# Kernel tuning notes

Hardware: AMD Instinct MI355X
Metric: run time of the kernel (lower is better)

Reference implementation:

```python
import jax, jax.numpy as jnp
import numpy as np

N_Q = 4       # n_qubits
PATCH = 3
PAD = 1       # patch_size // 2


def _u3(theta, phi, lam):
    # U3 gate matrix (2x2 complex)
    c = jnp.cos(theta / 2)
    s = jnp.sin(theta / 2)
    row0 = jnp.stack([c + 0j, -jnp.exp(1j * lam) * s])
    row1 = jnp.stack([jnp.exp(1j * phi) * s, jnp.exp(1j * (phi + lam)) * c])
    return jnp.stack([row0, row1]).astype(jnp.complex64)


def _apply_1q(state, U, wire):
    # state: (N,2,2,2,2) complex; U: (2,2) shared or (N,2,2) batched
    s = jnp.moveaxis(state, 1 + wire, -1)
    shp = s.shape
    s = s.reshape(s.shape[0], -1, 2)
    if U.ndim == 2:
        out = jnp.einsum('ij,nrj->nri', U, s)
    else:
        out = jnp.einsum('nij,nrj->nri', U, s)
    return jnp.moveaxis(out.reshape(shp), -1, 1 + wire)


def _apply_2q(state, U4, cw, tw):
    # U4: (4,4) on (control, target) subspace ordered |c t>
    s = jnp.moveaxis(state, (1 + cw, 1 + tw), (-2, -1))
    shp = s.shape
    s = s.reshape(s.shape[0], -1, 4)
    out = jnp.einsum('ij,nrj->nri', U4, s)
    return jnp.moveaxis(out.reshape(shp), (-2, -1), (1 + cw, 1 + tw))


def setup_inputs() -> dict:
    key = jax.random.key(0)
    ks = jax.random.split(key, 8)
    B, C, H, W = 16, 64, 64, 64
    out_ch = 128
    d_in = C * PATCH * PATCH  # 576
    x = jax.random.normal(ks[0], (B, C, H, W), dtype=jnp.float32)
    fc1_w = jax.random.normal(ks[1], (N_Q, d_in), dtype=jnp.float32) * (1.0 / np.sqrt(d_in))
    fc1_b = jax.random.normal(ks[2], (N_Q,), dtype=jnp.float32) * 0.01
    u3_params = jax.random.normal(ks[3], (N_Q, 3), dtype=jnp.float32)
    cu3_params = jax.random.normal(ks[4], (N_Q, 3), dtype=jnp.float32)
    fc_w = jax.random.normal(ks[5], (out_ch, N_Q), dtype=jnp.float32) * 0.5
    fc_b = jax.random.normal(ks[6], (out_ch,), dtype=jnp.float32) * 0.01
    return {"x": x, "fc1_w": fc1_w, "fc1_b": fc1_b, "u3_params": u3_params,
            "cu3_params": cu3_params, "fc_w": fc_w, "fc_b": fc_b}


def reference(x, fc1_w, fc1_b, u3_params, cu3_params, fc_w, fc_b):
    B, C, H, W = x.shape
    xp = jnp.pad(x, ((0, 0), (0, 0), (PAD, PAD), (PAD, PAD)))
    Hout, Wout = H, W  # stride 1, same padding
    # im2col: feature order (C, di, dj) matches torch patch.reshape(B,-1)
    cols = jnp.stack([xp[:, :, di:di + Hout, dj:dj + Wout]
                      for di in range(PATCH) for dj in range(PATCH)], axis=2)  # (B,C,9,H,W)
    patches = cols.transpose(0, 3, 4, 1, 2).reshape(B, Hout * Wout, C * PATCH * PATCH)
    ang = patches @ fc1_w.T + fc1_b  # (B, P, 4) rotation angles
    Np = B * Hout * Wout
    ang = ang.reshape(Np, N_Q)
    # initial state |0000> for every (batch, patch)
    state = jnp.zeros((Np, 2 ** N_Q), jnp.complex64).at[:, 0].set(1.0)
    state = state.reshape((Np,) + (2,) * N_Q)
    # RY encoding (per-element angles)
    for w in range(N_Q):
        th = ang[:, w] / 2
        c, s = jnp.cos(th), jnp.sin(th)
        Ury = jnp.stack([jnp.stack([c, -s], -1), jnp.stack([s, c], -1)], -2).astype(jnp.complex64)
        state = _apply_1q(state, Ury, w)
    # trainable U3 on every wire
    for w in range(N_Q):
        state = _apply_1q(state, _u3(u3_params[w, 0], u3_params[w, 1], u3_params[w, 2]), w)
    # circular CU3 ring (0,1),(1,2),(2,3),(3,0)
    for w in range(N_Q):
        U = _u3(cu3_params[w, 0], cu3_params[w, 1], cu3_params[w, 2])
        U4 = jnp.eye(4, dtype=jnp.complex64).at[2:, 2:].set(U)
        state = _apply_2q(state, U4, w, (w + 1) % N_Q)
    # <Z> on each wire
    probs = state.real ** 2 + state.imag ** 2  # (Np,2,2,2,2)
    zv = jnp.array([1.0, -1.0], jnp.float32)
    expz = jnp.stack(
        [(probs * zv.reshape((1,) + (1,) * w + (2,) + (1,) * (N_Q - 1 - w))).sum(axis=(1, 2, 3, 4))
         for w in range(N_Q)], axis=1)  # (Np,4)
    out = expz.reshape(B, Hout * Wout, N_Q) @ fc_w.T + fc_b  # (B,P,out_ch)
    out_ch = fc_w.shape[0]
    # faithful to original: view(B, out_ch, side_h, side_w) on contiguous (P,out_ch)
    return out.reshape(B, out_ch, Hout, Wout)
```

## Files before the change

### kernel.cpp

```cpp
#include <hip/hip_runtime.h>
#include <hip/hip_bf16.h>
#include <math.h>

typedef unsigned short u16;
typedef unsigned int   u32;
typedef unsigned long long u64;

#define WS_W2    0
#define WS_B4    2304
#define WS_FCW   2308
#define WS_FCB   2820
#define WS_GATES 2948
#define WS_FLAG  3012
#define WS_PART  4096

__device__ inline float bfbits2f(u32 lo16) {
    u32 u = lo16 << 16;
    return __builtin_bit_cast(float, u);
}
__device__ inline float bchi(u32 w) {
    return __builtin_bit_cast(float, w & 0xffff0000u);
}
__device__ inline float bclo(u32 w) {
    return __builtin_bit_cast(float, w << 16);
}
__device__ inline u16 f2bf(float f) {
    u32 u = __builtin_bit_cast(u32, f);
    u = u + 0x7fffu + ((u >> 16) & 1u);
    return (u16)(u >> 16);
}
__device__ inline float ld_param(const void* p, int i, int isbf16) {
    return isbf16 ? bfbits2f(((const u16*)p)[i]) : ((const float*)p)[i];
}

__global__ __launch_bounds__(256) void k0_prep(
        const void* __restrict__ x,
        const void* __restrict__ fc1_w, const void* __restrict__ fc1_b,
        const void* __restrict__ u3p,   const void* __restrict__ cu3p,
        const void* __restrict__ fc_w,  const void* __restrict__ fc_b,
        float* __restrict__ ws) {
    __shared__ int sflag;
    int t = threadIdx.x;
    if (t == 0) {
        const u32* xw = (const u32*)x;
        int cnt = 0;
        for (int i = 0; i < 64; ++i) {
            u32 e = (xw[i] >> 7) & 0xFFu;
            if (e >= 110 && e <= 130) ++cnt;
        }
        sflag = (cnt >= 32) ? 1 : 0;
        ws[WS_FLAG] = (float)sflag;
    }
    __syncthreads();
    const int bf = sflag;
    for (int idx = t; idx < 2304; idx += 256) {
        int c = idx / 36;
        int rem = idx - c * 36;
        int q = rem / 9;
        int k = rem - q * 9;
        ws[WS_W2 + idx] = ld_param(fc1_w, q * 576 + c * 9 + k, bf);
    }
    if (t < 4)   ws[WS_B4 + t] = ld_param(fc1_b, t, bf);
    for (int idx = t; idx < 512; idx += 256) ws[WS_FCW + idx] = ld_param(fc_w, idx, bf);
    if (t < 128) ws[WS_FCB + t] = ld_param(fc_b, t, bf);
    if (t < 8) {
        int w = t & 3;
        const void* p = (t < 4) ? u3p : cu3p;
        float th = ld_param(p, w * 3 + 0, bf);
        float ph = ld_param(p, w * 3 + 1, bf);
        float la = ld_param(p, w * 3 + 2, bf);
        float c = cosf(0.5f * th), s = sinf(0.5f * th);
        float cl = cosf(la), sl = sinf(la);
        float cp = cosf(ph), sp = sinf(ph);
        float cpl = cp * cl - sp * sl, spl = sp * cl + cp * sl;
        float* m = ws + WS_GATES + t * 8;
        m[0] = c;        m[1] = 0.f;
        m[2] = -cl * s;  m[3] = -sl * s;
        m[4] = cp * s;   m[5] = sp * s;
        m[6] = cpl * c;  m[7] = spl * c;
    }
}

__global__ __launch_bounds__(256) void kA_conv(
        const void* __restrict__ x, const float* __restrict__ ws,
        float4* __restrict__ part) {
    __shared__ u32 tile[3 * 16 * 34];
    __shared__ float4 red4[256];
    const int t = threadIdx.x;
    const int bid = blockIdx.x;
    const int cg  = bid & 3;
    const int row = (bid >> 2) & 63;
    const int b   = bid >> 8;
    const int bf = (ws[WS_FLAG] != 0.0f) ? 1 : 0;
    const int c0 = cg * 16;

    const u32*    xu = (const u32*)x;
    const float2* xf = (const float2*)x;
    const int xbase = b * 131072;

    {
        const int jj = t & 31;
        const int half = t >> 5;
#pragma unroll
        for (int i = 0; i < 6; ++i) {
            int rowcl = half + i * 8;
            int r = rowcl >> 4, cl = rowcl & 15;
            int gr = row - 1 + r;
            u32 pk = 0;
            if (gr >= 0 && gr < 64) {
                int idx = xbase + (c0 + cl) * 2048 + gr * 32 + jj;
                if (bf) pk = xu[idx];
                else { float2 v = xf[idx];
                       pk = (u32)f2bf(v.x) | ((u32)f2bf(v.y) << 16); }
            }
            tile[rowcl * 34 + 1 + jj] = pk;
        }
        if (t < 96) { int rc = t >> 1; tile[rc * 34 + ((t & 1) ? 33 : 0)] = 0u; }
    }
    __syncthreads();

    const int j = t & 63, tc = t >> 6;
    const int pj = (j + 1) >> 1;
    const int sh = (1 - (j & 1)) * 16;
    float ang0 = 0.f, ang1 = 0.f, ang2 = 0.f, ang3 = 0.f;
#pragma unroll
    for (int cc = 0; cc < 4; ++cc) {
        const int cl = tc * 4 + cc;
        const int cs = __builtin_amdgcn_readfirstlane(c0 + cl);
        const float* wp = ws + WS_W2 + cs * 36;
#pragma unroll
        for (int r = 0; r < 3; ++r) {
            const u32* rp = tile + (r * 16 + cl) * 34 + pj;
            u32 lo = rp[0], hi = rp[1];
            u64 v = (((u64)hi << 32) | lo) >> sh;
            u32 vlo = (u32)v, vhi = (u32)(v >> 32);
            float e0 = bclo(vlo);
            float e1 = bchi(vlo);
            float e2 = bclo(vhi);
            const float* w0 = wp + r * 3;
            ang0 += e0 * w0[0]  + e1 * w0[1]  + e2 * w0[2];
            ang1 += e0 * w0[9]  + e1 * w0[10] + e2 * w0[11];
            ang2 += e0 * w0[18] + e1 * w0[19] + e2 * w0[20];
            ang3 += e0 * w0[27] + e1 * w0[28] + e2 * w0[29];
        }
    }

    red4[tc * 64 + j] = make_float4(ang0, ang1, ang2, ang3);
    __syncthreads();
    if (t < 64) {
        float4 a0 = red4[t], a1 = red4[64 + t], a2 = red4[128 + t], a3 = red4[192 + t];
        float4 s = make_float4(a0.x + a1.x + a2.x + a3.x,
                               a0.y + a1.y + a2.y + a3.y,
                               a0.z + a1.z + a2.z + a3.z,
                               a0.w + a1.w + a2.w + a3.w);
        part[cg * 65536 + b * 4096 + row * 64 + t] = s;
    }
}

__global__ __launch_bounds__(256) void kB_circuit_fc(
        const float* __restrict__ ws, const float4* __restrict__ part,
        void* __restrict__ out) {
    __shared__ float4 smEz[64];
    const int t = threadIdx.x;
    const int bp0 = blockIdx.x * 64;
    const int bf = (ws[WS_FLAG] != 0.0f) ? 1 : 0;

    if (t < 64) {
        const int bp = bp0 + t;
        float4 a0 = part[bp];
        float4 a1 = part[65536 + bp];
        float4 a2 = part[131072 + bp];
        float4 a3 = part[196608 + bp];
        float angf[4];
        angf[0] = ws[WS_B4 + 0] + a0.x + a1.x + a2.x + a3.x;
        angf[1] = ws[WS_B4 + 1] + a0.y + a1.y + a2.y + a3.y;
        angf[2] = ws[WS_B4 + 2] + a0.z + a1.z + a2.z + a3.z;
        angf[3] = ws[WS_B4 + 3] + a0.w + a1.w + a2.w + a3.w;

        const float* G = ws + WS_GATES;
        float vr[4][2], vi[4][2];
#pragma unroll
        for (int w = 0; w < 4; ++w) {
            float sa, ca;
            __sincosf(0.5f * angf[w], &sa, &ca);
            const float* m = G + w * 8;
            vr[w][0] = m[0] * ca + m[2] * sa;  vi[w][0] = m[1] * ca + m[3] * sa;
            vr[w][1] = m[4] * ca + m[6] * sa;  vi[w][1] = m[5] * ca + m[7] * sa;
        }
        float t01r[4], t01i[4], t23r[4], t23i[4];
#pragma unroll
        for (int a = 0; a < 2; ++a)
#pragma unroll
            for (int bq = 0; bq < 2; ++bq) {
                t01r[a * 2 + bq] = vr[0][a] * vr[1][bq] - vi[0][a] * vi[1][bq];
                t01i[a * 2 + bq] = vr[0][a] * vi[1][bq] + vi[0][a] * vr[1][bq];
                t23r[a * 2 + bq] = vr[2][a] * vr[3][bq] - vi[2][a] * vi[3][bq];
                t23i[a * 2 + bq] = vr[2][a] * vi[3][bq] + vi[2][a] * vr[3][bq];
            }
        float ar[16], ai[16];
#pragma unroll
        for (int n = 0; n < 16; ++n) {
            int hi = n >> 2, lo = n & 3;
            ar[n] = t01r[hi] * t23r[lo] - t01i[hi] * t23i[lo];
            ai[n] = t01r[hi] * t23i[lo] + t01i[hi] * t23r[lo];
        }
#pragma unroll
        for (int w = 0; w < 4; ++w) {
            const float* m = G + 32 + w * 8;
            const int cb = 8 >> w;
            const int tb = 8 >> ((w + 1) & 3);
#pragma unroll
            for (int n = 0; n < 16; ++n) {
                if ((n & cb) != 0 && (n & tb) == 0) {
                    int n1 = n | tb;
                    float a0r = ar[n], a0i = ai[n], a1r = ar[n1], a1i = ai[n1];
                    ar[n]  = m[0] * a0r - m[1] * a0i + m[2] * a1r - m[3] * a1i;
                    ai[n]  = m[0] * a0i + m[1] * a0r + m[2] * a1i + m[3] * a1r;
                    ar[n1] = m[4] * a0r - m[5] * a0i + m[6] * a1r - m[7] * a1i;
                    ai[n1] = m[4] * a0i + m[5] * a0r + m[6] * a1i + m[7] * a1r;
                }
            }
        }
        float ez[4] = {0.f, 0.f, 0.f, 0.f};
#pragma unroll
        for (int n = 0; n < 16; ++n) {
            float pr = ar[n] * ar[n] + ai[n] * ai[n];
#pragma unroll
            for (int w = 0; w < 4; ++w)
                ez[w] += ((n >> (3 - w)) & 1) ? -pr : pr;
        }
        smEz[t] = make_float4(ez[0], ez[1], ez[2], ez[3]);
    }
    __syncthreads();

    const int og = (t & 15) * 8;
    const float4* fw4 = (const float4*)(ws + WS_FCW) + og;
    const float*  fbp = ws + WS_FCB + og;
    float4 w0 = fw4[0], w1 = fw4[1], w2 = fw4[2], w3 = fw4[3];
    float4 w4 = fw4[4], w5 = fw4[5], w6 = fw4[6], w7 = fw4[7];
    float4 bA = *(const float4*)fbp, bB = *(const float4*)(fbp + 4);
#pragma unroll
    for (int ch = 0; ch < 4; ++ch) {
        const int pl = (t >> 4) + ch * 16;
        const float4 ez = smEz[pl];
        float v0 = bA.x + ez.x*w0.x + ez.y*w0.y + ez.z*w0.z + ez.w*w0.w;
        float v1 = bA.y + ez.x*w1.x + ez.y*w1.y + ez.z*w1.z + ez.w*w1.w;
        float v2 = bA.z + ez.x*w2.x + ez.y*w2.y + ez.z*w2.z + ez.w*w2.w;
        float v3 = bA.w + ez.x*w3.x + ez.y*w3.y + ez.z*w3.z + ez.w*w3.w;
        float v4 = bB.x + ez.x*w4.x + ez.y*w4.y + ez.z*w4.z + ez.w*w4.w;
        float v5 = bB.y + ez.x*w5.x + ez.y*w5.y + ez.z*w5.z + ez.w*w5.w;
        float v6 = bB.z + ez.x*w6.x + ez.y*w6.y + ez.z*w6.z + ez.w*w6.w;
        float v7 = bB.w + ez.x*w7.x + ez.y*w7.y + ez.z*w7.z + ez.w*w7.w;
        if (bf) {
            u32 p0 = (u32)f2bf(v0) | ((u32)f2bf(v1) << 16);
            u32 p1 = (u32)f2bf(v2) | ((u32)f2bf(v3) << 16);
            u32 p2 = (u32)f2bf(v4) | ((u32)f2bf(v5) << 16);
            u32 p3 = (u32)f2bf(v6) | ((u32)f2bf(v7) << 16);
            ((uint4*)out)[blockIdx.x * 1024 + ch * 256 + t] =
                make_uint4(p0, p1, p2, p3);
        } else {
            float4* o = (float4*)out + (blockIdx.x * 2048 + ch * 512 + 2 * t);
            o[0] = make_float4(v0, v1, v2, v3);
            o[1] = make_float4(v4, v5, v6, v7);
        }
    }
}

extern "C" void kernel_launch(void* const* d_in, const int* in_sizes, int n_in,
                              void* d_out, int out_size, void* d_ws, size_t ws_size,
                              hipStream_t stream) {
    float* ws = (float*)d_ws;
    float4* part = (float4*)(ws + WS_PART);
    k0_prep<<<dim3(1), dim3(256), 0, stream>>>(d_in[0], d_in[1], d_in[2], d_in[3],
                                               d_in[4], d_in[5], d_in[6], ws);
    kA_conv<<<dim3(4096), dim3(256), 0, stream>>>(d_in[0], ws, part);
    kB_circuit_fc<<<dim3(1024), dim3(256), 0, stream>>>(ws, part, d_out);
}
```

Measured before the change: 110.8 us.

## Split conv over 8 channel groups and preload packed bf16 weights into registers

The conv kernel now uses 8 channel groups of 8 channels instead of 4 groups of 16, so it launches twice as many blocks, each with a smaller shared tile. The fc1 weights are repacked as bf16 pairs in the prep kernel and each thread preloads its 36 packed words into registers, replacing the per-iteration float loads. The circuit kernel reduces 8 partial sums instead of 4. This raises parallelism and cuts weight load traffic, but doubles the partial-sum workspace traffic, adds register pressure, and rounds the weights to bf16, which may cost precision.

```diff
diff --git a/kernel.cpp b/kernel.cpp
--- a/kernel.cpp
+++ b/kernel.cpp
@@ -53,12 +53,18 @@
     }
     __syncthreads();
     const int bf = sflag;
-    for (int idx = t; idx < 2304; idx += 256) {
-        int c = idx / 36;
-        int rem = idx - c * 36;
-        int q = rem / 9;
-        int k = rem - q * 9;
-        ws[WS_W2 + idx] = ld_param(fc1_w, q * 576 + c * 9 + k, bf);
+    u32* wpk = (u32*)ws + WS_W2;
+    for (int idx = t; idx < 1152; idx += 256) {
+        int c = idx / 18;
+        int rem = idx - c * 18;
+        int r = rem / 6;
+        int p = rem - r * 6;
+        int i0 = 2 * p, i1 = 2 * p + 1;
+        int q0 = i0 / 3, d0 = i0 - 3 * q0;
+        int q1 = i1 / 3, d1 = i1 - 3 * q1;
+        u32 lo = f2bf(ld_param(fc1_w, q0 * 576 + c * 9 + r * 3 + d0, bf));
+        u32 hi = f2bf(ld_param(fc1_w, q1 * 576 + c * 9 + r * 3 + d1, bf));
+        wpk[idx] = lo | (hi << 16);
     }
     if (t < 4)   ws[WS_B4 + t] = ld_param(fc1_b, t, bf);
     for (int idx = t; idx < 512; idx += 256) ws[WS_FCW + idx] = ld_param(fc_w, idx, bf);
@@ -84,15 +90,22 @@
 __global__ __launch_bounds__(256) void kA_conv(
         const void* __restrict__ x, const float* __restrict__ ws,
         float4* __restrict__ part) {
-    __shared__ u32 tile[3 * 16 * 34];
+    __shared__ u32 tile[24 * 34];
     __shared__ float4 red4[256];
     const int t = threadIdx.x;
     const int bid = blockIdx.x;
-    const int cg  = bid & 3;
-    const int row = (bid >> 2) & 63;
-    const int b   = bid >> 8;
+    const int cg  = bid & 7;
+    const int row = (bid >> 3) & 63;
+    const int b   = bid >> 9;
     const int bf = (ws[WS_FLAG] != 0.0f) ? 1 : 0;
-    const int c0 = cg * 16;
+    const int c0 = cg * 8;
+    const int tc = t >> 6;
+
+    const int cs = __builtin_amdgcn_readfirstlane(c0 + tc * 2);
+    const u32* wpk = (const u32*)ws + WS_W2 + cs * 18;
+    u32 w36[36];
+#pragma unroll
+    for (int i = 0; i < 36; ++i) w36[i] = wpk[i];
 
     const u32*    xu = (const u32*)x;
     const float2* xf = (const float2*)x;
@@ -100,11 +113,11 @@
 
     {
         const int jj = t & 31;
-        const int half = t >> 5;
-#pragma unroll
-        for (int i = 0; i < 6; ++i) {
-            int rowcl = half + i * 8;
-            int r = rowcl >> 4, cl = rowcl & 15;
+        const int g8 = t >> 5;
+#pragma unroll
+        for (int i = 0; i < 3; ++i) {
+            int rowcl = g8 + i * 8;
+            int r = rowcl >> 3, cl = rowcl & 7;
             int gr = row - 1 + r;
             u32 pk = 0;
             if (gr >= 0 && gr < 64) {
@@ -115,33 +128,33 @@
             }
             tile[rowcl * 34 + 1 + jj] = pk;
         }
-        if (t < 96) { int rc = t >> 1; tile[rc * 34 + ((t & 1) ? 33 : 0)] = 0u; }
-    }
-    __syncthreads();
-
-    const int j = t & 63, tc = t >> 6;
+        if (t < 48) { int rc = t >> 1; tile[rc * 34 + ((t & 1) ? 33 : 0)] = 0u; }
+    }
+    __syncthreads();
+
+    const int j = t & 63;
     const int pj = (j + 1) >> 1;
     const int sh = (1 - (j & 1)) * 16;
     float ang0 = 0.f, ang1 = 0.f, ang2 = 0.f, ang3 = 0.f;
 #pragma unroll
-    for (int cc = 0; cc < 4; ++cc) {
-        const int cl = tc * 4 + cc;
-        const int cs = __builtin_amdgcn_readfirstlane(c0 + cl);
-        const float* wp = ws + WS_W2 + cs * 36;
+    for (int cc = 0; cc < 2; ++cc) {
+        const int cl = tc * 2 + cc;
 #pragma unroll
         for (int r = 0; r < 3; ++r) {
-            const u32* rp = tile + (r * 16 + cl) * 34 + pj;
+            const u32* rp = tile + (r * 8 + cl) * 34 + pj;
             u32 lo = rp[0], hi = rp[1];
             u64 v = (((u64)hi << 32) | lo) >> sh;
             u32 vlo = (u32)v, vhi = (u32)(v >> 32);
             float e0 = bclo(vlo);
             float e1 = bchi(vlo);
             float e2 = bclo(vhi);
-            const float* w0 = wp + r * 3;
-            ang0 += e0 * w0[0]  + e1 * w0[1]  + e2 * w0[2];
-            ang1 += e0 * w0[9]  + e1 * w0[10] + e2 * w0[11];
-            ang2 += e0 * w0[18] + e1 * w0[19] + e2 * w0[20];
-            ang3 += e0 * w0[27] + e1 * w0[28] + e2 * w0[29];
+            const int wb = cc * 18 + r * 6;
+            u32 u0 = w36[wb], u1 = w36[wb + 1], u2 = w36[wb + 2];
+            u32 u3 = w36[wb + 3], u4 = w36[wb + 4], u5 = w36[wb + 5];
+            ang0 += e0 * bclo(u0) + e1 * bchi(u0) + e2 * bclo(u1);
+            ang1 += e0 * bchi(u1) + e1 * bclo(u2) + e2 * bchi(u2);
+            ang2 += e0 * bclo(u3) + e1 * bchi(u3) + e2 * bclo(u4);
+            ang3 += e0 * bchi(u4) + e1 * bclo(u5) + e2 * bchi(u5);
         }
     }
 
@@ -167,15 +180,17 @@
 
     if (t < 64) {
         const int bp = bp0 + t;
-        float4 a0 = part[bp];
-        float4 a1 = part[65536 + bp];
-        float4 a2 = part[131072 + bp];
-        float4 a3 = part[196608 + bp];
+        float ax = 0.f, ay = 0.f, az = 0.f, aw = 0.f;
+#pragma unroll
+        for (int g = 0; g < 8; ++g) {
+            float4 a = part[g * 65536 + bp];
+            ax += a.x; ay += a.y; az += a.z; aw += a.w;
+        }
         float angf[4];
-        angf[0] = ws[WS_B4 + 0] + a0.x + a1.x + a2.x + a3.x;
-        angf[1] = ws[WS_B4 + 1] + a0.y + a1.y + a2.y + a3.y;
-        angf[2] = ws[WS_B4 + 2] + a0.z + a1.z + a2.z + a3.z;
-        angf[3] = ws[WS_B4 + 3] + a0.w + a1.w + a2.w + a3.w;
+        angf[0] = ws[WS_B4 + 0] + ax;
+        angf[1] = ws[WS_B4 + 1] + ay;
+        angf[2] = ws[WS_B4 + 2] + az;
+        angf[3] = ws[WS_B4 + 3] + aw;
 
         const float* G = ws + WS_GATES;
         float vr[4][2], vi[4][2];
@@ -273,6 +288,6 @@
     float4* part = (float4*)(ws + WS_PART);
     k0_prep<<<dim3(1), dim3(256), 0, stream>>>(d_in[0], d_in[1], d_in[2], d_in[3],
                                                d_in[4], d_in[5], d_in[6], ws);
-    kA_conv<<<dim3(4096), dim3(256), 0, stream>>>(d_in[0], ws, part);
+    kA_conv<<<dim3(8192), dim3(256), 0, stream>>>(d_in[0], ws, part);
     kB_circuit_fc<<<dim3(1024), dim3(256), 0, stream>>>(ws, part, d_out);
 }
```

After: 108.6 us. 2.0% less time.
